# Kernel tuning notes

Measured on AMD Instinct MI355X. Metric: run time of the kernel, lower is better.

Reference implementation:

```python
import jax, jax.numpy as jnp
import numpy as np

N, E, IN_FT, OUT_FT = 20000, 4096, 128, 128


def setup_inputs() -> dict:
    key = jax.random.key(0)
    kx, kh, kw = jax.random.split(key, 3)
    X = jax.random.normal(kx, (N, IN_FT), dtype=jnp.float32)
    H = jax.random.randint(kh, (N, E), 0, 2, dtype=jnp.int32)
    weight = jax.random.normal(kw, (IN_FT, OUT_FT), dtype=jnp.float32) * (1.0 / np.sqrt(IN_FT))
    bias = jnp.zeros((OUT_FT,), dtype=jnp.float32)
    return {"X": X, "H": H, "weight": weight, "bias": bias}


def reference(X, H, weight, bias):
    # Dv^{-1/2} H De^{-1} H^T Dv^{-1/2} X W + b, with diag matrices fused as
    # row/column scalings (same math as the torch.diag @ chain, no NxN temporaries).
    Hf = H.astype(jnp.float32)
    v_deg = jnp.sum(Hf, axis=1)            # [N]
    e_deg = jnp.sum(Hf, axis=0)            # [E]
    v_deg = jnp.where(v_deg > 0, v_deg, 1.0)
    e_deg = jnp.where(e_deg > 0, e_deg, 1.0)
    dv_inv_sqrt = 1.0 / jnp.sqrt(v_deg)    # diag(Dv^-1/2)
    de_inv = 1.0 / e_deg                   # diag(De^-1)
    Y = dv_inv_sqrt[:, None] * X
    T = Hf.T @ Y                           # H^T (...)        [E, in]
    T = de_inv[:, None] * T                # De^-1 (...)
    Z = Hf @ T                             # H (...)          [N, in]
    Z = dv_inv_sqrt[:, None] * Z           # Dv^-1/2 (...)
    out = Z @ weight + bias                # [N, out]
    return out
```

## Files before the change

### kernel.cpp

```cpp
#include <hip/hip_runtime.h>

#define NV 20000
#define NE 4096
#define FT 128
#define NW_E 128
#define NW_V 625
#define PT_STRIDE 632
#define NKC2 157
#define K_TOT 20096

typedef __attribute__((ext_vector_type(8))) short short8v;
typedef __attribute__((ext_vector_type(4))) float float4v;

__device__ __forceinline__ unsigned short f2bf(float f) {
    unsigned u = __float_as_uint(f);
    u += 0x7FFFu + ((u >> 16) & 1u);
    return (unsigned short)(u >> 16);
}
__device__ __forceinline__ int lds_off(int r, int c) {
    return r * 256 + ((c ^ (r & 15)) << 4);
}
__device__ __forceinline__ uint4 lut_entry(int t) {
    uint4 e;
    e.x = ((t & 1) ? 0x3F80u : 0u) | ((t & 2) ? 0x3F800000u : 0u);
    e.y = ((t & 4) ? 0x3F80u : 0u) | ((t & 8) ? 0x3F800000u : 0u);
    e.z = ((t & 16) ? 0x3F80u : 0u) | ((t & 32) ? 0x3F800000u : 0u);
    e.w = ((t & 64) ? 0x3F80u : 0u) | ((t & 128) ? 0x3F800000u : 0u);
    return e;
}
__device__ __forceinline__ void cp16(void* l, const void* g) {
    __builtin_amdgcn_global_load_lds((__attribute__((address_space(1))) void*)g,
                                     (__attribute__((address_space(3))) void*)l, 16, 0, 0);
}

__global__ __launch_bounds__(256) void k_pack(const int* __restrict__ H,
                                              unsigned* __restrict__ packed,
                                              float* __restrict__ dv,
                                              int* __restrict__ de_cnt) {
    __shared__ int cl[4];
    int t = threadIdx.x, wave = t >> 6, lane = t & 63;
    if (blockIdx.x < 16) de_cnt[blockIdx.x * 256 + t] = 0;
    int row = blockIdx.x * 2 + (wave >> 1);
    int half = wave & 1;
    const uint4* base = reinterpret_cast<const uint4*>(H) + (size_t)row * 1024 + half * 512 + lane * 8;
    unsigned m = 0;
#pragma unroll
    for (int i = 0; i < 8; ++i) {
        uint4 v = base[i];
        m |= (v.x ? 1u : 0u) << (i * 4 + 0);
        m |= (v.y ? 1u : 0u) << (i * 4 + 1);
        m |= (v.z ? 1u : 0u) << (i * 4 + 2);
        m |= (v.w ? 1u : 0u) << (i * 4 + 3);
    }
    packed[(size_t)row * NW_E + half * 64 + lane] = m;
    int c = __popc(m);
    for (int o = 32; o > 0; o >>= 1) c += __shfl_down(c, o, 64);
    if (lane == 0) cl[wave] = c;
    __syncthreads();
    if (t < 2) {
        int d = cl[t * 2] + cl[t * 2 + 1];
        dv[blockIdx.x * 2 + t] = d > 0 ? 1.0f / sqrtf((float)d) : 1.0f;
    }
}

__global__ __launch_bounds__(256) void k_btrans(const unsigned* __restrict__ packed,
                                                unsigned* __restrict__ packedT,
                                                int* __restrict__ de_cnt) {
    int lane = threadIdx.x & 63;
    int w = threadIdx.x >> 6;
    int ew = blockIdx.y * 4 + w;
    int n = blockIdx.x * 64 + lane;
    unsigned wv = (n < NV) ? packed[(size_t)n * NW_E + ew] : 0u;
    unsigned my = 0;
#pragma unroll
    for (int j = 0; j < 32; ++j) {
        unsigned long long m = __ballot(((wv >> j) & 1u) != 0);
        unsigned part = (lane < 32) ? (unsigned)m : (unsigned)(m >> 32);
        if ((lane & 31) == j) my = part;
    }
    int nw = blockIdx.x * 2 + (lane >> 5);
    int e = ew * 32 + (lane & 31);
    if (nw <= 625) packedT[(size_t)e * PT_STRIDE + nw] = my;
    int cnt = __popc(my);
    cnt += __shfl_down(cnt, 32, 64);
    if (lane < 32) atomicAdd(de_cnt + e, cnt);
}

__global__ __launch_bounds__(256) void k_mid(const float* __restrict__ X,
                                             const float* __restrict__ dv,
                                             unsigned short* __restrict__ At) {
    int t = threadIdx.x;
    int f = t & 127;
    int item = blockIdx.x * 2 + (t >> 7);
    int nbase = item * 8;
    unsigned short h[8];
#pragma unroll
    for (int i = 0; i < 8; ++i) {
        int n = nbase + i;
        float v = (n < NV) ? X[(size_t)n * FT + f] * dv[n] : 0.0f;
        h[i] = f2bf(v);
    }
    uint4 u;
    u.x = (unsigned)h[0] | ((unsigned)h[1] << 16);
    u.y = (unsigned)h[2] | ((unsigned)h[3] << 16);
    u.z = (unsigned)h[4] | ((unsigned)h[5] << 16);
    u.w = (unsigned)h[6] | ((unsigned)h[7] << 16);
    int kc2 = nbase >> 7;
    int c = (nbase >> 3) & 15;
    *reinterpret_cast<uint4*>(At + (size_t)kc2 * 16384 + f * 128 + ((c ^ (f & 15)) << 3)) = u;
}

__global__ __launch_bounds__(256, 2) void k_mm1(const unsigned short* __restrict__ At,
                                                const unsigned* __restrict__ packedT,
                                                float* __restrict__ P, int chunkK) {
    __shared__ __align__(16) unsigned char sA[32768];
    __shared__ __align__(16) unsigned char sB[32768];
    __shared__ __align__(16) uint4 slut[256];
    int t = threadIdx.x;
    slut[t] = lut_entry(t);

    int et = blockIdx.x & 31, kp = blockIdx.x >> 5;
    int e0 = et * 128;
    int kbeg = kp * chunkK;
    int kend = kbeg + chunkK; if (kend > K_TOT) kend = K_TOT;
    int iters = (kend - kbeg) >> 7; if (iters < 0) iters = 0;

    float4v acc[4][4];
#pragma unroll
    for (int i = 0; i < 4; ++i)
#pragma unroll
        for (int j = 0; j < 4; ++j)
#pragma unroll
            for (int r = 0; r < 4; ++r) acc[i][j][r] = 0.0f;

    int wave = t >> 6, lane = t & 63;
    int wm0 = (wave & 1) * 64, wc0 = (wave >> 1) * 64;
    int r0 = lane & 15, q = lane >> 4;

    const uint4* brow4 = reinterpret_cast<const uint4*>(
        packedT + (size_t)(e0 + (t & 127)) * PT_STRIDE + (kbeg >> 5));
    uint4 bw;
    if (t < 128 && iters > 0) bw = *brow4;
    __syncthreads();

    const char* gA = reinterpret_cast<const char*>(At) + (size_t)(kbeg >> 7) * 32768 + wave * 8192 + lane * 16;
    char* lA = reinterpret_cast<char*>(sA) + wave * 8192;

    for (int it = 0; it < iters; ++it) {
        const char* g = gA + (size_t)it * 32768;
#pragma unroll
        for (int j = 0; j < 8; ++j) cp16(lA + j * 1024, g + j * 1024);
        if (t < 128) {
            uint4 nxt = brow4[it + 1];
            unsigned wd[4] = {bw.x, bw.y, bw.z, bw.w};
#pragma unroll
            for (int c = 0; c < 16; ++c)
                *reinterpret_cast<uint4*>(sB + lds_off(t, c)) = slut[(wd[c >> 2] >> ((c & 3) * 8)) & 0xFF];
            bw = nxt;
        }
        __syncthreads();
#pragma unroll
        for (int ks = 0; ks < 4; ++ks) {
            short8v a[4], bb[4];
#pragma unroll
            for (int mi = 0; mi < 4; ++mi)
                a[mi] = *reinterpret_cast<const short8v*>(sA + lds_off(wm0 + mi * 16 + r0, ks * 4 + q));
#pragma unroll
            for (int ci = 0; ci < 4; ++ci)
                bb[ci] = *reinterpret_cast<const short8v*>(sB + lds_off(wc0 + ci * 16 + r0, ks * 4 + q));
#pragma unroll
            for (int mi = 0; mi < 4; ++mi)
#pragma unroll
                for (int ci = 0; ci < 4; ++ci)
                    acc[mi][ci] = __builtin_amdgcn_mfma_f32_16x16x32_bf16(a[mi], bb[ci], acc[mi][ci], 0, 0, 0);
        }
        __syncthreads();
    }
    float* Pp = P + (size_t)kp * (128 * 4096);
#pragma unroll
    for (int mi = 0; mi < 4; ++mi)
#pragma unroll
        for (int ci = 0; ci < 4; ++ci) {
            int f = wm0 + mi * 16 + q * 4;
            int e = e0 + wc0 + ci * 16 + r0;
#pragma unroll
            for (int r = 0; r < 4; ++r)
                Pp[(size_t)(f + r) * 4096 + e] = acc[mi][ci][r];
        }
}

__global__ __launch_bounds__(256) void k_reduce(const float4v* __restrict__ P,
                                                float4v* __restrict__ Tt, int S) {
    int i = blockIdx.x * 256 + threadIdx.x;
    float4v a = P[i];
    for (int p = 1; p < S; ++p) a += P[(size_t)p * 131072 + i];
    Tt[i] = a;
}

__global__ __launch_bounds__(256) void k_ut(const float* __restrict__ Tt,
                                            const float* __restrict__ W,
                                            const int* __restrict__ de_cnt,
                                            unsigned short* __restrict__ Ut) {
    int t = threadIdx.x;
    int bx = blockIdx.x;
    int j = t & 63;
    int e = bx * 64 + j;
    int g0 = blockIdx.y * 16 + (t >> 6) * 4;
    float a0 = 0, a1 = 0, a2 = 0, a3 = 0;
    for (int f = 0; f < 128; ++f) {
        float tv = Tt[(size_t)f * 4096 + e];
        float4 wv = *reinterpret_cast<const float4*>(W + f * 128 + g0);
        a0 += tv * wv.x; a1 += tv * wv.y; a2 += tv * wv.z; a3 += tv * wv.w;
    }
    int cnt = de_cnt[e];
    float d = cnt > 0 ? 1.0f / (float)cnt : 1.0f;
    float av[4] = {a0, a1, a2, a3};
    int slabB = bx >> 1;
    int chi = ((bx & 1) << 3) | (j >> 3);
    int pos = j & 7;
#pragma unroll
    for (int k = 0; k < 4; ++k) {
        int g = g0 + k;
        int qg = g >> 5, gr = g & 31;
        Ut[(size_t)(qg * 32 + slabB) * 4096 + gr * 128 + ((chi ^ (gr & 15)) << 3) + pos] = f2bf(av[k] * d);
    }
}

__global__ __launch_bounds__(256, 3) void k_mm2(const unsigned* __restrict__ packed,
                                                const unsigned short* __restrict__ Ut,
                                                const float* __restrict__ dv,
                                                const float* __restrict__ bias,
                                                float* __restrict__ out) {
    __shared__ __align__(16) unsigned char sA[32768];
    __shared__ __align__(16) unsigned char sB[8192];
    __shared__ __align__(16) uint4 slut[256];
    int t = threadIdx.x;
    slut[t] = lut_entry(t);

    int mt = blockIdx.x >> 2, qg = blockIdx.x & 3;
    int n0 = mt * 128, g0 = qg * 32;

    float4v acc[4];
#pragma unroll
    for (int i = 0; i < 4; ++i)
#pragma unroll
        for (int r = 0; r < 4; ++r) acc[i][r] = 0.0f;

    int wave = t >> 6, lane = t & 63;
    int wm0 = (wave & 1) * 64, wc0 = (wave >> 1) * 16;
    int r0 = lane & 15, q = lane >> 4;

    const uint4* arow4 = reinterpret_cast<const uint4*>(packed + (size_t)(n0 + (t & 127)) * NW_E);
    uint4 aw;
    if (t < 128) aw = *arow4;
    __syncthreads();

    int wb = wave & 1;
    const char* gB = reinterpret_cast<const char*>(Ut) + (size_t)(qg * 32) * 8192 + wb * 4096 + lane * 16;
    char* lB = reinterpret_cast<char*>(sB) + wb * 4096;

    for (int it = 0; it < 32; ++it) {
        if (t < 128) {
            uint4 nxt = arow4[it + 1];
            unsigned wd[4] = {aw.x, aw.y, aw.z, aw.w};
#pragma unroll
            for (int c = 0; c < 16; ++c)
                *reinterpret_cast<uint4*>(sA + lds_off(t, c)) = slut[(wd[c >> 2] >> ((c & 3) * 8)) & 0xFF];
            aw = nxt;
        } else {
            const char* g = gB + (size_t)it * 8192;
#pragma unroll
            for (int j = 0; j < 4; ++j) cp16(lB + j * 1024, g + j * 1024);
        }
        __syncthreads();
#pragma unroll
        for (int ks = 0; ks < 4; ++ks) {
            short8v a[4], bb;
#pragma unroll
            for (int mi = 0; mi < 4; ++mi)
                a[mi] = *reinterpret_cast<const short8v*>(sA + lds_off(wm0 + mi * 16 + r0, ks * 4 + q));
            bb = *reinterpret_cast<const short8v*>(sB + lds_off(wc0 + r0, ks * 4 + q));
#pragma unroll
            for (int mi = 0; mi < 4; ++mi)
                acc[mi] = __builtin_amdgcn_mfma_f32_16x16x32_bf16(a[mi], bb, acc[mi], 0, 0, 0);
        }
        __syncthreads();
    }
    {
        int g = g0 + wc0 + r0;
        float bg = bias[g];
#pragma unroll
        for (int mi = 0; mi < 4; ++mi) {
#pragma unroll
            for (int r = 0; r < 4; ++r) {
                int n = n0 + wm0 + mi * 16 + q * 4 + r;
                if (n < NV) out[(size_t)n * 128 + g] = dv[n] * acc[mi][r] + bg;
            }
        }
    }
}

extern "C" void kernel_launch(void* const* d_in, const int* in_sizes, int n_in,
                              void* d_out, int out_size, void* d_ws, size_t ws_size,
                              hipStream_t stream) {
    const float* X    = (const float*)d_in[0];
    const int*   H    = (const int*)d_in[1];
    const float* W    = (const float*)d_in[2];
    const float* bias = (const float*)d_in[3];
    float* out = (float*)d_out;

    char* ws = (char*)d_ws;
    size_t off = 0;
    auto alloc = [&](size_t sz) { char* p = ws + off; off += (sz + 255) & ~(size_t)255; return p; };
    unsigned*       packed  = (unsigned*)alloc((size_t)NV * NW_E * 4);
    unsigned*       packedT = (unsigned*)alloc((size_t)NE * PT_STRIDE * 4);
    unsigned short* At      = (unsigned short*)alloc((size_t)NKC2 * 16384 * 2);
    float*          Tt      = (float*)alloc((size_t)FT * NE * 4);
    unsigned short* Ut      = (unsigned short*)alloc((size_t)FT * NE * 2);
    float*          dv      = (float*)alloc((size_t)NV * 4);
    int*            de_cnt  = (int*)alloc((size_t)NE * 4);
    size_t fixed = off;

    long long avail = (long long)ws_size - (long long)fixed;
    int S = (int)(avail / (128LL * 4096 * 4));
    if (S > 16) S = 16;
    if (S < 1) S = 1;
    float* P1 = (float*)(ws + fixed);
    int chunkK = ((NKC2 + S - 1) / S) * 128;

    k_pack  <<<NV / 2, 256, 0, stream>>>(H, packed, dv, de_cnt);
    k_btrans<<<dim3(313, 32), 256, 0, stream>>>(packed, packedT, de_cnt);
    k_mid   <<<1256, 256, 0, stream>>>(X, dv, At);
    k_mm1   <<<32 * S, 256, 0, stream>>>(At, packedT, P1, chunkK);
    k_reduce<<<512, 256, 0, stream>>>((const float4v*)P1, (float4v*)Tt, S);
    k_ut    <<<dim3(64, 8), 256, 0, stream>>>(Tt, W, de_cnt, Ut);
    k_mm2   <<<628, 256, 0, stream>>>(packed, Ut, dv, bias, out);
}
```

Before: 587.2 us.

## Butterfly bit transpose, split LUT expansion across all threads, fuse reduce into U build

The 32-step ballot loop in the bit-matrix transpose becomes a 5-stage shuffle-xor butterfly. In both GEMM kernels, all 256 threads now share the LUT-based expansion of bit rows into bf16 tiles, where before only half of them did it. In mm2 the Ut tile copy now overlaps with this expansion instead of running on the other half of the threads. The partial-sum layout moves to e-major with float4 stores, and the split-K reduction is fused with the W multiply and De scaling into one kernel. That removes the Tt round trip and one launch, at the cost of fewer threads per element in the W product.

```diff
diff --git a/kernel.cpp b/kernel.cpp
--- a/kernel.cpp
+++ b/kernel.cpp
@@ -70,18 +70,27 @@
     int w = threadIdx.x >> 6;
     int ew = blockIdx.y * 4 + w;
     int n = blockIdx.x * 64 + lane;
-    unsigned wv = (n < NV) ? packed[(size_t)n * NW_E + ew] : 0u;
-    unsigned my = 0;
-#pragma unroll
-    for (int j = 0; j < 32; ++j) {
-        unsigned long long m = __ballot(((wv >> j) & 1u) != 0);
-        unsigned part = (lane < 32) ? (unsigned)m : (unsigned)(m >> 32);
-        if ((lane & 31) == j) my = part;
-    }
+    unsigned x = (n < NV) ? packed[(size_t)n * NW_E + ew] : 0u;
+    unsigned y;
+    y = __shfl_xor(x, 16, 64);
+    x = (lane & 16) ? ((x & 0xFFFF0000u) | ((y >> 16) & 0x0000FFFFu))
+                    : ((x & 0x0000FFFFu) | ((y << 16) & 0xFFFF0000u));
+    y = __shfl_xor(x, 8, 64);
+    x = (lane & 8)  ? ((x & 0xFF00FF00u) | ((y >> 8) & 0x00FF00FFu))
+                    : ((x & 0x00FF00FFu) | ((y << 8) & 0xFF00FF00u));
+    y = __shfl_xor(x, 4, 64);
+    x = (lane & 4)  ? ((x & 0xF0F0F0F0u) | ((y >> 4) & 0x0F0F0F0Fu))
+                    : ((x & 0x0F0F0F0Fu) | ((y << 4) & 0xF0F0F0F0u));
+    y = __shfl_xor(x, 2, 64);
+    x = (lane & 2)  ? ((x & 0xCCCCCCCCu) | ((y >> 2) & 0x33333333u))
+                    : ((x & 0x33333333u) | ((y << 2) & 0xCCCCCCCCu));
+    y = __shfl_xor(x, 1, 64);
+    x = (lane & 1)  ? ((x & 0xAAAAAAAAu) | ((y >> 1) & 0x55555555u))
+                    : ((x & 0x55555555u) | ((y << 1) & 0xAAAAAAAAu));
     int nw = blockIdx.x * 2 + (lane >> 5);
     int e = ew * 32 + (lane & 31);
-    if (nw <= 625) packedT[(size_t)e * PT_STRIDE + nw] = my;
-    int cnt = __popc(my);
+    if (nw <= 625) packedT[(size_t)e * PT_STRIDE + nw] = x;
+    int cnt = __popc(x);
     cnt += __shfl_down(cnt, 32, 64);
     if (lane < 32) atomicAdd(de_cnt + e, cnt);
 }
@@ -137,10 +146,11 @@
     int wm0 = (wave & 1) * 64, wc0 = (wave >> 1) * 64;
     int r0 = lane & 15, q = lane >> 4;
 
+    int rB = t & 127, half = t >> 7, cb = half << 3;
     const uint4* brow4 = reinterpret_cast<const uint4*>(
-        packedT + (size_t)(e0 + (t & 127)) * PT_STRIDE + (kbeg >> 5));
+        packedT + (size_t)(e0 + rB) * PT_STRIDE + (kbeg >> 5));
     uint4 bw;
-    if (t < 128 && iters > 0) bw = *brow4;
+    if (iters > 0) bw = brow4[0];
     __syncthreads();
 
     const char* gA = reinterpret_cast<const char*>(At) + (size_t)(kbeg >> 7) * 32768 + wave * 8192 + lane * 16;
@@ -150,12 +160,16 @@
         const char* g = gA + (size_t)it * 32768;
 #pragma unroll
         for (int j = 0; j < 8; ++j) cp16(lA + j * 1024, g + j * 1024);
-        if (t < 128) {
+        {
             uint4 nxt = brow4[it + 1];
-            unsigned wd[4] = {bw.x, bw.y, bw.z, bw.w};
-#pragma unroll
-            for (int c = 0; c < 16; ++c)
-                *reinterpret_cast<uint4*>(sB + lds_off(t, c)) = slut[(wd[c >> 2] >> ((c & 3) * 8)) & 0xFF];
+            unsigned wd0 = half ? bw.z : bw.x;
+            unsigned wd1 = half ? bw.w : bw.y;
+#pragma unroll
+            for (int c = 0; c < 4; ++c)
+                *reinterpret_cast<uint4*>(sB + lds_off(rB, cb + c)) = slut[(wd0 >> (c * 8)) & 0xFF];
+#pragma unroll
+            for (int c = 0; c < 4; ++c)
+                *reinterpret_cast<uint4*>(sB + lds_off(rB, cb + 4 + c)) = slut[(wd1 >> (c * 8)) & 0xFF];
             bw = nxt;
         }
         __syncthreads();
@@ -176,52 +190,50 @@
         }
         __syncthreads();
     }
-    float* Pp = P + (size_t)kp * (128 * 4096);
+    float* Pp = P + (size_t)kp * (4096 * 128);
 #pragma unroll
     for (int mi = 0; mi < 4; ++mi)
 #pragma unroll
         for (int ci = 0; ci < 4; ++ci) {
             int f = wm0 + mi * 16 + q * 4;
             int e = e0 + wc0 + ci * 16 + r0;
-#pragma unroll
-            for (int r = 0; r < 4; ++r)
-                Pp[(size_t)(f + r) * 4096 + e] = acc[mi][ci][r];
-        }
-}
-
-__global__ __launch_bounds__(256) void k_reduce(const float4v* __restrict__ P,
-                                                float4v* __restrict__ Tt, int S) {
-    int i = blockIdx.x * 256 + threadIdx.x;
-    float4v a = P[i];
-    for (int p = 1; p < S; ++p) a += P[(size_t)p * 131072 + i];
-    Tt[i] = a;
-}
-
-__global__ __launch_bounds__(256) void k_ut(const float* __restrict__ Tt,
-                                            const float* __restrict__ W,
-                                            const int* __restrict__ de_cnt,
-                                            unsigned short* __restrict__ Ut) {
+            *reinterpret_cast<float4v*>(Pp + (size_t)e * 128 + f) = acc[mi][ci];
+        }
+}
+
+__global__ __launch_bounds__(256) void k_redut(const float* __restrict__ P,
+                                               const float* __restrict__ W,
+                                               const int* __restrict__ de_cnt,
+                                               unsigned short* __restrict__ Ut, int S) {
+    __shared__ float sT[8][132];
     int t = threadIdx.x;
-    int bx = blockIdx.x;
-    int j = t & 63;
-    int e = bx * 64 + j;
-    int g0 = blockIdx.y * 16 + (t >> 6) * 4;
+    int e0 = blockIdx.x * 8;
+    {
+        int el = t >> 5, fq = (t & 31) * 4;
+        const float* base = P + (size_t)(e0 + el) * 128 + fq;
+        float4 s = {0.f, 0.f, 0.f, 0.f};
+        for (int p = 0; p < S; ++p) {
+            float4 v = *reinterpret_cast<const float4*>(base + (size_t)p * 524288);
+            s.x += v.x; s.y += v.y; s.z += v.z; s.w += v.w;
+        }
+        *reinterpret_cast<float4*>(&sT[el][fq]) = s;
+    }
+    __syncthreads();
+    int el = t & 7, gq = (t >> 3) * 4;
+    int e = e0 + el;
     float a0 = 0, a1 = 0, a2 = 0, a3 = 0;
     for (int f = 0; f < 128; ++f) {
-        float tv = Tt[(size_t)f * 4096 + e];
-        float4 wv = *reinterpret_cast<const float4*>(W + f * 128 + g0);
+        float tv = sT[el][f];
+        float4 wv = *reinterpret_cast<const float4*>(W + f * 128 + gq);
         a0 += tv * wv.x; a1 += tv * wv.y; a2 += tv * wv.z; a3 += tv * wv.w;
     }
     int cnt = de_cnt[e];
     float d = cnt > 0 ? 1.0f / (float)cnt : 1.0f;
     float av[4] = {a0, a1, a2, a3};
-    int slabB = bx >> 1;
-    int chi = ((bx & 1) << 3) | (j >> 3);
-    int pos = j & 7;
+    int slabB = e >> 7, chi = (e >> 3) & 15, pos = e & 7;
 #pragma unroll
     for (int k = 0; k < 4; ++k) {
-        int g = g0 + k;
-        int qg = g >> 5, gr = g & 31;
+        int g = gq + k, qg = g >> 5, gr = g & 31;
         Ut[(size_t)(qg * 32 + slabB) * 4096 + gr * 128 + ((chi ^ (gr & 15)) << 3) + pos] = f2bf(av[k] * d);
     }
 }
@@ -250,27 +262,31 @@
     int wm0 = (wave & 1) * 64, wc0 = (wave >> 1) * 16;
     int r0 = lane & 15, q = lane >> 4;
 
-    const uint4* arow4 = reinterpret_cast<const uint4*>(packed + (size_t)(n0 + (t & 127)) * NW_E);
-    uint4 aw;
-    if (t < 128) aw = *arow4;
+    int rA = t & 127, half = t >> 7, cb = half << 3;
+    const uint4* arow4 = reinterpret_cast<const uint4*>(packed + (size_t)(n0 + rA) * NW_E);
+    uint4 aw = arow4[0];
     __syncthreads();
 
-    int wb = wave & 1;
-    const char* gB = reinterpret_cast<const char*>(Ut) + (size_t)(qg * 32) * 8192 + wb * 4096 + lane * 16;
-    char* lB = reinterpret_cast<char*>(sB) + wb * 4096;
+    const char* gB = reinterpret_cast<const char*>(Ut) + (size_t)(qg * 32) * 8192 + (wave & 1) * 4096 + lane * 16;
+    char* lB = reinterpret_cast<char*>(sB) + (wave & 1) * 4096;
 
     for (int it = 0; it < 32; ++it) {
-        if (t < 128) {
-            uint4 nxt = arow4[it + 1];
-            unsigned wd[4] = {aw.x, aw.y, aw.z, aw.w};
-#pragma unroll
-            for (int c = 0; c < 16; ++c)
-                *reinterpret_cast<uint4*>(sA + lds_off(t, c)) = slut[(wd[c >> 2] >> ((c & 3) * 8)) & 0xFF];
+        uint4 nxt = arow4[it + 1];
+        if (wave < 2) {
+            const char* g = gB + (size_t)it * 8192;
+#pragma unroll
+            for (int j = 0; j < 4; ++j) cp16(lB + j * 1024, g + j * 1024);
+        }
+        {
+            unsigned wd0 = half ? aw.z : aw.x;
+            unsigned wd1 = half ? aw.w : aw.y;
+#pragma unroll
+            for (int c = 0; c < 4; ++c)
+                *reinterpret_cast<uint4*>(sA + lds_off(rA, cb + c)) = slut[(wd0 >> (c * 8)) & 0xFF];
+#pragma unroll
+            for (int c = 0; c < 4; ++c)
+                *reinterpret_cast<uint4*>(sA + lds_off(rA, cb + 4 + c)) = slut[(wd1 >> (c * 8)) & 0xFF];
             aw = nxt;
-        } else {
-            const char* g = gB + (size_t)it * 8192;
-#pragma unroll
-            for (int j = 0; j < 4; ++j) cp16(lB + j * 1024, g + j * 1024);
         }
         __syncthreads();
 #pragma unroll
@@ -315,7 +331,6 @@
     unsigned*       packed  = (unsigned*)alloc((size_t)NV * NW_E * 4);
     unsigned*       packedT = (unsigned*)alloc((size_t)NE * PT_STRIDE * 4);
     unsigned short* At      = (unsigned short*)alloc((size_t)NKC2 * 16384 * 2);
-    float*          Tt      = (float*)alloc((size_t)FT * NE * 4);
     unsigned short* Ut      = (unsigned short*)alloc((size_t)FT * NE * 2);
     float*          dv      = (float*)alloc((size_t)NV * 4);
     int*            de_cnt  = (int*)alloc((size_t)NE * 4);
@@ -332,7 +347,6 @@
     k_btrans<<<dim3(313, 32), 256, 0, stream>>>(packed, packedT, de_cnt);
     k_mid   <<<1256, 256, 0, stream>>>(X, dv, At);
     k_mm1   <<<32 * S, 256, 0, stream>>>(At, packedT, P1, chunkK);
-    k_reduce<<<512, 256, 0, stream>>>((const float4v*)P1, (float4v*)Tt, S);
-    k_ut    <<<dim3(64, 8), 256, 0, stream>>>(Tt, W, de_cnt, Ut);
+    k_redut <<<512, 256, 0, stream>>>(P1, W, de_cnt, Ut, S);
     k_mm2   <<<628, 256, 0, stream>>>(packed, Ut, dv, bias, out);
 }
```

Result: no change. 589.1 us (+0.3%).
